# Kernel optimization log

Hardware: AMD Instinct MI355X
Metric: run time of the kernel (lower is better)

## Reference

```python
import jax, jax.numpy as jnp
import numpy as np

B, W, N, K = 8, 16, 40, 10
DN = DL = 128
DE = 128
H = 4
NEG_SLOPE = 0.2


def _build_graph():
    # per-graph ring adjacency: i -> (i+d) % N for d=1..K, in dense_to_sparse order (src-major, dst ascending)
    src0, dst0 = [], []
    for i in range(N):
        ds = sorted(((i + d) % N) for d in range(1, K + 1))
        src0 += [i] * K
        dst0 += ds
    src0 = np.asarray(src0)
    dst0 = np.asarray(dst0)
    G = B * W
    Epg = N * K
    offs = np.arange(G)[:, None] * N
    node_adj = np.stack([(src0[None] + offs).reshape(-1), (dst0[None] + offs).reshape(-1)])
    # line graph: for each node, pair every incoming edge with every outgoing edge (torch repeat/tile order)
    a0, a1, fe = [], [], []
    for num in range(N):
        inc = np.nonzero(dst0 == num)[0]
        out = np.nonzero(src0 == num)[0]
        a0.append(np.repeat(inc, out.size))
        a1.append(np.tile(out, inc.size))
        fe.append(np.full(inc.size * out.size, num))
    a0, a1, fe = np.concatenate(a0), np.concatenate(a1), np.concatenate(fe)
    keep = a0 != a1  # remove_self_loops (no-op here, kept for fidelity)
    a0, a1, fe = a0[keep], a1[keep], fe[keep]
    eoffs = np.arange(G)[:, None] * Epg
    edge_adj = np.stack([(a0[None] + eoffs).reshape(-1), (a1[None] + eoffs).reshape(-1)])
    edge_efea = (fe[None] + offs).reshape(-1)
    return node_adj, edge_adj, edge_efea


def setup_inputs() -> dict:
    key = jax.random.key(0)
    node_adj, edge_adj, edge_efea = _build_graph()
    Epg = N * K
    D1 = DN + DL
    ks = jax.random.split(key, 16)

    def lin(k, fi, fo):
        return jax.random.normal(k, (fi, fo), jnp.float32) / np.sqrt(fi).astype(np.float32)

    return dict(
        x_node=jax.random.normal(ks[0], (B, W, N, DN), jnp.float32),
        x_trace=jax.random.normal(ks[1], (B, W, Epg, DE), jnp.float32),
        x_log=jax.random.normal(ks[2], (B, W, N, DL), jnp.float32),
        node_adj=jnp.asarray(node_adj, jnp.int32),
        edge_adj=jnp.asarray(edge_adj, jnp.int32),
        edge_efea=jnp.asarray(edge_efea, jnp.int32),
        Wl1=lin(ks[3], D1, D1), bl1=jnp.zeros((D1,), jnp.float32),
        Wr1=lin(ks[4], D1, D1), br1=jnp.zeros((D1,), jnp.float32),
        We1=lin(ks[5], DE, D1), be1=jnp.zeros((D1,), jnp.float32),
        att1=jax.random.normal(ks[6], (H, D1 // H), jnp.float32) / np.sqrt(D1 // H).astype(np.float32),
        bias1=jnp.zeros((D1,), jnp.float32),
        Wl2=lin(ks[7], DE, DE), bl2=jnp.zeros((DE,), jnp.float32),
        Wr2=lin(ks[8], DE, DE), br2=jnp.zeros((DE,), jnp.float32),
        We2=lin(ks[9], D1, DE), be2=jnp.zeros((DE,), jnp.float32),
        att2=jax.random.normal(ks[10], (H, DE // H), jnp.float32) / np.sqrt(DE // H).astype(np.float32),
        bias2=jnp.zeros((DE,), jnp.float32),
    )


def _gatv2(x, edge_index, edge_attr, Wl, bl, Wr, br, We, be, att, bias, heads):
    """PyG GATv2Conv (eval mode, add_self_loops=False, concat heads)."""
    n = x.shape[0]
    HC = Wl.shape[1]
    C = HC // heads
    xl = (x @ Wl + bl).reshape(n, heads, C)  # source transform
    xr = (x @ Wr + br).reshape(n, heads, C)  # target transform
    src, dst = edge_index[0], edge_index[1]
    ea = (edge_attr @ We + be).reshape(-1, heads, C)
    m = jax.nn.leaky_relu(xl[src] + xr[dst] + ea, NEG_SLOPE)  # [E,H,C]
    logits = jnp.einsum('ehc,hc->eh', m, att)
    # segment softmax over incoming edges per target node
    mx = jax.ops.segment_max(logits, dst, num_segments=n)
    mx = jnp.where(jnp.isfinite(mx), mx, 0.0)
    ex = jnp.exp(logits - mx[dst])
    den = jax.ops.segment_sum(ex, dst, num_segments=n)
    alpha = ex / (den[dst] + 1e-16)
    out = jax.ops.segment_sum(alpha[:, :, None] * xl[src], dst, num_segments=n)  # [n,H,C]
    return out.reshape(n, HC) + bias


def reference(x_node, x_trace, x_log, node_adj, edge_adj, edge_efea,
              Wl1, bl1, Wr1, br1, We1, be1, att1, bias1,
              Wl2, bl2, Wr2, br2, We2, be2, att2, bias2):
    b, w, n, dn = x_node.shape
    dl = x_log.shape[-1]
    node = jnp.concatenate([x_node, x_log], axis=-1).reshape(-1, dn + dl)  # [G*N, Dn+Dl]
    trace = x_trace.reshape(-1, x_trace.shape[-1])                          # [G*Epg, De]
    node = _gatv2(node, node_adj, trace, Wl1, bl1, Wr1, br1, We1, be1, att1, bias1, H)
    trace = _gatv2(trace, edge_adj, node[edge_efea], Wl2, bl2, Wr2, br2, We2, be2, att2, bias2, H)
    x_node_o = node[:, :dn].reshape(b, w, n, dn)
    x_trace_o = trace.reshape(b, w, -1, trace.shape[-1])
    x_log_o = node[:, dn:].reshape(b, w, n, dl)
    return (x_node_o, x_trace_o, x_log_o)
```

## Files before the change

kernel.cpp:

```cpp
#include <hip/hip_runtime.h>
#include <hip/hip_bf16.h>

#define D1 256
#define DE 128
#define KDEG 10
#define LOG2E 1.44269504088896340736f

typedef __attribute__((ext_vector_type(8))) short short8;
typedef __attribute__((ext_vector_type(4))) float f32x4;

static inline int cdiv(size_t a, int b) { return (int)((a + b - 1) / b); }
static inline size_t al256(size_t x) { return (x + 255) & ~(size_t)255; }

__device__ __forceinline__ short f2b(float x) {
  __hip_bfloat16 h = __float2bfloat16(x);
  return *reinterpret_cast<short*>(&h);
}

__global__ __launch_bounds__(256) void k_setup(const float* __restrict__ xn,
                                               const float* __restrict__ xlg,
                                               const float* __restrict__ Wl1,
                                               const float* __restrict__ Wr1,
                                               const float* __restrict__ We1,
                                               const float* __restrict__ Wl2,
                                               const float* __restrict__ Wr2,
                                               const float* __restrict__ We2,
                                               const float* __restrict__ bl1,
                                               const float* __restrict__ br1,
                                               float* __restrict__ den1,
                                               int* __restrict__ cnt,
                                               float* __restrict__ X,
                                               short* __restrict__ WT12,
                                               short* __restrict__ We1T,
                                               short* __restrict__ W2T,
                                               short* __restrict__ We2T,
                                               float* __restrict__ blr1,
                                               int NN) {
  size_t idx = (size_t)blockIdx.x * 256 + threadIdx.x;
  size_t n;
  n = (size_t)NN * 4;       if (idx < n) { den1[idx] = 0.f; return; }           idx -= n;
  n = (size_t)NN;           if (idx < n) { cnt[idx] = 0; return; }              idx -= n;
  n = (size_t)NN * D1;
  if (idx < n) {
    int g = (int)(idx >> 8), c = (int)(idx & 255);
    X[idx] = (c < 128) ? xn[(size_t)g * 128 + c] : xlg[(size_t)g * 128 + (c - 128)];
    return;
  }
  idx -= n;
  n = 512 * 256;
  if (idx < n) {
    int nn = (int)(idx >> 8), k = (int)(idx & 255);
    float v = (nn < 256) ? Wl1[(size_t)k * 256 + nn] : Wr1[(size_t)k * 256 + (nn - 256)];
    WT12[idx] = f2b(v);
    return;
  }
  idx -= n;
  n = 256 * 128;
  if (idx < n) {
    int nn = (int)(idx >> 7), k = (int)(idx & 127);
    We1T[idx] = f2b(We1[(size_t)k * 256 + nn]);
    return;
  }
  idx -= n;
  n = 2 * 128 * 128;
  if (idx < n) {
    int half = (int)(idx >> 14);
    int r = (int)(idx & 16383);
    int nn = r >> 7, k = r & 127;
    const float* W = half ? Wr2 : Wl2;
    W2T[idx] = f2b(W[(size_t)k * 128 + nn]);
    return;
  }
  idx -= n;
  n = 128 * 256;
  if (idx < n) {
    int nn = (int)(idx >> 8), k = (int)(idx & 255);
    We2T[idx] = f2b(We2[(size_t)k * 128 + nn]);
    return;
  }
  idx -= n;
  n = 512;
  if (idx < n) blr1[idx] = (idx < 256) ? bl1[idx] : br1[idx - 256];
}

__global__ __launch_bounds__(256) void k_build_inc(const int* __restrict__ adj,
                                                   int* __restrict__ cnt,
                                                   int* __restrict__ inc, int NE) {
  int e = blockIdx.x * 256 + threadIdx.x;
  if (e >= NE) return;
  int dst = adj[NE + e];
  int slot = atomicAdd(&cnt[dst], 1);
  inc[dst * KDEG + slot] = e;
}

__global__ __launch_bounds__(256) void k_gemm_mfma(const float* __restrict__ A,
                                                   const short* __restrict__ WT,
                                                   const float* __restrict__ bias,
                                                   float* __restrict__ C,
                                                   int M, int K, int N) {
  __shared__ __align__(16) short As[128][40];
  __shared__ __align__(16) short Bs[128][40];
  const int tid = threadIdx.x;
  const int wave = tid >> 6, lane = tid & 63;
  const int quad = lane >> 4, l16 = lane & 15;
  const int m0 = blockIdx.y * 128, n0 = blockIdx.x * 128;
  const int wm = (wave & 1) * 64, wn = (wave >> 1) * 64;
  f32x4 acc[4][4] = {};
  for (int k0 = 0; k0 < K; k0 += 32) {
    #pragma unroll
    for (int s = 0; s < 2; ++s) {
      int ch = tid + s * 256;
      int r = ch >> 2, kc = (ch & 3) << 3;
      const float* src = &A[(size_t)(m0 + r) * K + (k0 + kc)];
      float4 v0 = *(const float4*)src;
      float4 v1 = *(const float4*)(src + 4);
      short8 t;
      t[0] = f2b(v0.x); t[1] = f2b(v0.y); t[2] = f2b(v0.z); t[3] = f2b(v0.w);
      t[4] = f2b(v1.x); t[5] = f2b(v1.y); t[6] = f2b(v1.z); t[7] = f2b(v1.w);
      *(short8*)&As[r][kc] = t;
      *(short8*)&Bs[r][kc] = *(const short8*)&WT[(size_t)(n0 + r) * K + (k0 + kc)];
    }
    __syncthreads();
    short8 af[4], bf[4];
    #pragma unroll
    for (int mt = 0; mt < 4; ++mt)
      af[mt] = *(const short8*)&As[wm + mt * 16 + l16][quad << 3];
    #pragma unroll
    for (int nt = 0; nt < 4; ++nt)
      bf[nt] = *(const short8*)&Bs[wn + nt * 16 + l16][quad << 3];
    #pragma unroll
    for (int mt = 0; mt < 4; ++mt)
      #pragma unroll
      for (int nt = 0; nt < 4; ++nt)
        acc[mt][nt] = __builtin_amdgcn_mfma_f32_16x16x32_bf16(
            af[mt], bf[nt], acc[mt][nt], 0, 0, 0);
    __syncthreads();
  }
  #pragma unroll
  for (int nt = 0; nt < 4; ++nt) {
    int col = n0 + wn + nt * 16 + l16;
    float bs = bias[col];
    #pragma unroll
    for (int mt = 0; mt < 4; ++mt) {
      int row = m0 + wm + mt * 16 + (quad << 2);
      #pragma unroll
      for (int r = 0; r < 4; ++r)
        C[(size_t)(row + r) * N + col] = acc[mt][nt][r] + bs;
    }
  }
}

__global__ __launch_bounds__(256) void k_gemm_mfma64(const float* __restrict__ A,
                                                     const short* __restrict__ WT,
                                                     const float* __restrict__ bias,
                                                     float* __restrict__ C,
                                                     int M, int K, int N) {
  __shared__ __align__(16) short As[64][40];
  __shared__ __align__(16) short Bs[64][40];
  const int tid = threadIdx.x;
  const int wave = tid >> 6, lane = tid & 63;
  const int quad = lane >> 4, l16 = lane & 15;
  const int m0 = blockIdx.y * 64, n0 = blockIdx.x * 64;
  const int wm = (wave & 1) * 32, wn = (wave >> 1) * 32;
  f32x4 acc[2][2] = {};
  for (int k0 = 0; k0 < K; k0 += 32) {
    {
      int r = tid >> 2, kc = (tid & 3) << 3;
      const float* src = &A[(size_t)(m0 + r) * K + (k0 + kc)];
      float4 v0 = *(const float4*)src;
      float4 v1 = *(const float4*)(src + 4);
      short8 t;
      t[0] = f2b(v0.x); t[1] = f2b(v0.y); t[2] = f2b(v0.z); t[3] = f2b(v0.w);
      t[4] = f2b(v1.x); t[5] = f2b(v1.y); t[6] = f2b(v1.z); t[7] = f2b(v1.w);
      *(short8*)&As[r][kc] = t;
      *(short8*)&Bs[r][kc] = *(const short8*)&WT[(size_t)(n0 + r) * K + (k0 + kc)];
    }
    __syncthreads();
    short8 af[2], bf[2];
    #pragma unroll
    for (int mt = 0; mt < 2; ++mt)
      af[mt] = *(const short8*)&As[wm + mt * 16 + l16][quad << 3];
    #pragma unroll
    for (int nt = 0; nt < 2; ++nt)
      bf[nt] = *(const short8*)&Bs[wn + nt * 16 + l16][quad << 3];
    #pragma unroll
    for (int mt = 0; mt < 2; ++mt)
      #pragma unroll
      for (int nt = 0; nt < 2; ++nt)
        acc[mt][nt] = __builtin_amdgcn_mfma_f32_16x16x32_bf16(
            af[mt], bf[nt], acc[mt][nt], 0, 0, 0);
    __syncthreads();
  }
  #pragma unroll
  for (int nt = 0; nt < 2; ++nt) {
    int col = n0 + wn + nt * 16 + l16;
    float bs = bias[col];
    #pragma unroll
    for (int mt = 0; mt < 2; ++mt) {
      int row = m0 + wm + mt * 16 + (quad << 2);
      #pragma unroll
      for (int r = 0; r < 4; ++r)
        C[(size_t)(row + r) * N + col] = acc[mt][nt][r] + bs;
    }
  }
}

__global__ __launch_bounds__(256) void k_logit1_lite(const int* __restrict__ adj,
                                                     const float* __restrict__ ea,
                                                     const float* __restrict__ xlr1,
                                                     const float* __restrict__ att1,
                                                     float* __restrict__ logit1,
                                                     float* __restrict__ den1,
                                                     int NE, int e0) {
  int eb = e0 + blockIdx.x * 8;
  int c = threadIdx.x;
  __shared__ int sd[8][2];
  if (c < 8)       sd[c][0] = adj[eb + c];
  else if (c < 16) sd[c - 8][1] = adj[NE + eb + (c - 8)];
  __syncthreads();
  int h = c >> 6;
  float att = att1[c] * LOG2E;
  #pragma unroll
  for (int j = 0; j < 8; ++j) {
    int s = sd[j][0], d = sd[j][1];
    float v = xlr1[(size_t)s * 512 + c] + xlr1[(size_t)d * 512 + 256 + c]
            + ea[(size_t)(eb - e0 + j) * D1 + c];
    v = (v > 0.f) ? v : 0.2f * v;
    float p = v * att;
    #pragma unroll
    for (int m = 32; m >= 1; m >>= 1) p += __shfl_xor(p, m, 64);
    if ((c & 63) == 0) {
      float ex = exp2f(p);
      logit1[(size_t)(eb + j) * 4 + h] = ex;
      atomicAdd(&den1[(size_t)d * 4 + h], ex);
    }
  }
}

__global__ __launch_bounds__(256) void k_agg1(const int* __restrict__ adj,
                                              const int* __restrict__ inc,
                                              const float* __restrict__ xlr1,
                                              const float* __restrict__ logit1,
                                              const float* __restrict__ den1,
                                              const float* __restrict__ bias1,
                                              float* __restrict__ nodeout,
                                              float* __restrict__ out_node,
                                              float* __restrict__ out_log) {
  int u = blockIdx.x, c = threadIdx.x;
  __shared__ int se[KDEG], ssrc[KDEG];
  __shared__ float slg[KDEG * 4];
  if (c < KDEG) se[c] = inc[u * KDEG + c];
  __syncthreads();
  if (c < KDEG) ssrc[c] = adj[se[c]];
  else if (c >= 64 && c < 64 + KDEG * 4) {
    int t = c - 64;
    slg[t] = logit1[(size_t)se[t >> 2] * 4 + (t & 3)];
  }
  __syncthreads();
  int h = c >> 6;
  float rden = 1.f / (den1[(size_t)u * 4 + h] + 1e-16f);
  float acc = 0.f;
  #pragma unroll
  for (int j = 0; j < KDEG; ++j)
    acc += slg[j * 4 + h] * xlr1[(size_t)ssrc[j] * 512 + c];
  float val = acc * rden + bias1[c];
  nodeout[(size_t)u * D1 + c] = val;
  if (c < 128) out_node[(size_t)u * 128 + c] = val;
  else         out_log[(size_t)u * 128 + (c - 128)] = val;
}

__global__ __launch_bounds__(256) void k_gat2_v3(const int* __restrict__ eadj,
                                                 const int* __restrict__ efea,
                                                 const float* __restrict__ xl2,
                                                 const float* __restrict__ nproj,
                                                 const float* __restrict__ att2,
                                                 const float* __restrict__ bias2,
                                                 float* trace,
                                                 int NL, int g0, int e0) {
  int gi = g0 + blockIdx.x;
  size_t le0 = (size_t)gi * 100;
  int t = threadIdx.x;
  __shared__ int ein[KDEG], eout[KDEG], nvs;
  __shared__ float xs[KDEG][132];
  __shared__ float rs[KDEG][132];
  __shared__ float as_[DE];
  __shared__ float exs[400];
  __shared__ float rdn[40];
  if (t < KDEG)          ein[t] = eadj[le0 + (size_t)t * KDEG];
  else if (t < 2 * KDEG) eout[t - KDEG] = eadj[(size_t)NL + le0 + (t - KDEG)];
  else if (t == 255)     nvs = efea[le0];
  __syncthreads();
  int nv = nvs;
  for (int s = t; s < 320; s += 256) {
    int j = s >> 5, q = (s & 31) << 2;
    *(float4*)&xs[j][q] = *(const float4*)&xl2[(size_t)(ein[j] - e0) * DE + q];
    float4 tr4 = *(const float4*)&trace[(size_t)eout[j] * DE + q];
    float4 ea4 = *(const float4*)&nproj[(size_t)nv * DE + q];
    float4 r;
    r.x = tr4.x + ea4.x; r.y = tr4.y + ea4.y;
    r.z = tr4.z + ea4.z; r.w = tr4.w + ea4.w;
    *(float4*)&rs[j][q] = r;
  }
  if (t < 32) {
    float4 a4 = *(const float4*)&att2[t << 2];
    float4 o;
    o.x = a4.x * LOG2E; o.y = a4.y * LOG2E;
    o.z = a4.z * LOG2E; o.w = a4.w * LOG2E;
    *(float4*)&as_[t << 2] = o;
  }
  __syncthreads();
  for (int s = t; s < 400; s += 256) {
    int h = s & 3;
    int j = s / 40;
    int o = (s - j * 40) >> 2;
    const float* xa = &xs[j][h << 5];
    const float* ra = &rs[o][h << 5];
    const float* aa = &as_[h << 5];
    float p = 0.f;
    #pragma unroll
    for (int i = 0; i < 32; i += 4) {
      float4 xv = *(const float4*)&xa[i];
      float4 rv = *(const float4*)&ra[i];
      float4 av = *(const float4*)&aa[i];
      float v;
      v = xv.x + rv.x; v = (v > 0.f) ? v : 0.2f * v; p += v * av.x;
      v = xv.y + rv.y; v = (v > 0.f) ? v : 0.2f * v; p += v * av.y;
      v = xv.z + rv.z; v = (v > 0.f) ? v : 0.2f * v; p += v * av.z;
      v = xv.w + rv.w; v = (v > 0.f) ? v : 0.2f * v; p += v * av.w;
    }
    exs[s] = exp2f(p);
  }
  __syncthreads();
  if (t < 40) {
    float d = 0.f;
    #pragma unroll
    for (int j = 0; j < KDEG; ++j) d += exs[(j * 10 + (t >> 2)) * 4 + (t & 3)];
    rdn[t] = 1.f / d;
  }
  __syncthreads();
  {
    int c = t & 127, h = c >> 5, oh = (t >> 7) * 5;
    float bsv = bias2[c];
    #pragma unroll
    for (int oo = 0; oo < 5; ++oo) {
      int o = oh + oo;
      float acc = 0.f;
      #pragma unroll
      for (int j = 0; j < KDEG; ++j)
        acc += exs[(j * 10 + o) * 4 + h] * xs[j][c];
      trace[(size_t)eout[o] * DE + c] = acc * rdn[o * 4 + h] + bsv;
    }
  }
}

extern "C" void kernel_launch(void* const* d_in, const int* in_sizes, int n_in,
                              void* d_out, int out_size, void* d_ws, size_t ws_size,
                              hipStream_t stream) {
  const float* x_node   = (const float*)d_in[0];
  const float* x_trace  = (const float*)d_in[1];
  const float* x_log    = (const float*)d_in[2];
  const int*   node_adj = (const int*)d_in[3];
  const int*   edge_adj = (const int*)d_in[4];
  const int*   edge_efea= (const int*)d_in[5];
  const float* Wl1 = (const float*)d_in[6];
  const float* bl1 = (const float*)d_in[7];
  const float* Wr1 = (const float*)d_in[8];
  const float* br1 = (const float*)d_in[9];
  const float* We1 = (const float*)d_in[10];
  const float* be1 = (const float*)d_in[11];
  const float* att1 = (const float*)d_in[12];
  const float* bias1 = (const float*)d_in[13];
  const float* Wl2 = (const float*)d_in[14];
  const float* bl2 = (const float*)d_in[15];
  const float* Wr2 = (const float*)d_in[16];
  const float* br2 = (const float*)d_in[17];
  const float* We2 = (const float*)d_in[18];
  const float* be2 = (const float*)d_in[19];
  const float* att2 = (const float*)d_in[20];
  const float* bias2 = (const float*)d_in[21];

  const int NN = in_sizes[0] / 128;
  const int NE = in_sizes[1] / 128;
  const int NL = in_sizes[5];

  size_t sz_xlr1  = al256((size_t)NN * 512 * 4);
  size_t sz_log1  = al256((size_t)NE * 4 * 4);
  size_t sz_den1  = al256((size_t)NN * 4 * 4);
  size_t sz_nproj = al256((size_t)NN * DE * 4);
  size_t sz_inc   = al256((size_t)NN * KDEG * 4);
  size_t sz_cnt   = al256((size_t)NN * 4);
  size_t sz_wt12  = al256((size_t)512 * 256 * 2);
  size_t sz_we1t  = al256((size_t)256 * 128 * 2);
  size_t sz_w2t   = al256((size_t)2 * 128 * 128 * 2);
  size_t sz_we2t  = al256((size_t)128 * 256 * 2);
  size_t sz_blr1  = al256(512 * 4);
  size_t tail = sz_xlr1 + sz_log1 + sz_den1 + sz_nproj + sz_inc + sz_cnt +
                sz_wt12 + sz_we1t + sz_w2t + sz_we2t + sz_blr1;
  char* tb = (char*)d_ws + ((ws_size - tail) & ~(size_t)255);
  float* xlr1   = (float*)tb;  tb += sz_xlr1;
  float* logit1 = (float*)tb;  tb += sz_log1;
  float* den1   = (float*)tb;  tb += sz_den1;
  float* nproj  = (float*)tb;  tb += sz_nproj;
  int*   inc    = (int*)tb;    tb += sz_inc;
  int*   cnt    = (int*)tb;    tb += sz_cnt;
  short* WT12   = (short*)tb;  tb += sz_wt12;
  short* We1T   = (short*)tb;  tb += sz_we1t;
  short* W2T    = (short*)tb;  tb += sz_w2t;
  short* We2T   = (short*)tb;  tb += sz_we2t;
  float* blr1   = (float*)tb;
  short* Wl2T = W2T, *Wr2T = W2T + (size_t)128 * 128;

  float* pool    = (float*)d_ws;
  float* X       = pool;
  float* nodeout = pool;
  size_t pool_avail = (size_t)((char*)d_ws + ((ws_size - tail) & ~(size_t)255) - (char*)d_ws);

  int p1 = 16, p2 = 16;
  for (int q = 1; q <= 16; q <<= 1)
    if (((size_t)NE / q) * D1 * 4 <= pool_avail) { p1 = q; break; }
  for (int q = 1; q <= 16; q <<= 1)
    if (((size_t)NE / q) * DE * 4 <= pool_avail) { p2 = q; break; }

  float* out_node  = (float*)d_out;
  float* out_trace = out_node + (size_t)NN * 128;
  float* out_log   = out_trace + (size_t)NE * 128;

  {
    size_t total = (size_t)NN * 5 + (size_t)NN * D1 + 512 * 256 + 256 * 128 +
                   2 * 128 * 128 + 128 * 256 + 512;
    k_setup<<<cdiv(total, 256), 256, 0, stream>>>(x_node, x_log, Wl1, Wr1, We1,
                                                  Wl2, Wr2, We2, bl1, br1,
                                                  den1, cnt, X, WT12, We1T, W2T,
                                                  We2T, blr1, NN);
  }
  k_build_inc<<<cdiv(NE, 256), 256, 0, stream>>>(node_adj, cnt, inc, NE);

  k_gemm_mfma<<<dim3(512 / 128, NN / 128), 256, 0, stream>>>(X, WT12, blr1, xlr1,
                                                             NN, D1, 512);
  {
    int ep = NE / p1;
    for (int q = 0; q < p1; ++q) {
      const float* At = x_trace + (size_t)q * ep * DE;
      k_gemm_mfma<<<dim3(D1 / 128, ep / 128), 256, 0, stream>>>(At, We1T, be1, pool,
                                                                ep, DE, D1);
      k_logit1_lite<<<ep / 8, 256, 0, stream>>>(node_adj, pool, xlr1, att1,
                                                logit1, den1, NE, q * ep);
    }
  }

  k_agg1<<<NN, 256, 0, stream>>>(node_adj, inc, xlr1, logit1, den1, bias1,
                                 nodeout, out_node, out_log);

  k_gemm_mfma64<<<dim3(DE / 64, NN / 64), 256, 0, stream>>>(nodeout, We2T, be2,
                                                            nproj, NN, D1, DE);
  k_gemm_mfma<<<dim3(DE / 128, NE / 128), 256, 0, stream>>>(x_trace, Wr2T, br2,
                                                            out_trace, NE, DE, DE);
  {
    int ep = NE / p2, gp = NN / p2;
    for (int q = 0; q < p2; ++q) {
      const float* At = x_trace + (size_t)q * ep * DE;
      k_gemm_mfma<<<dim3(DE / 128, ep / 128), 256, 0, stream>>>(At, Wl2T, bl2, pool,
                                                                ep, DE, DE);
      k_gat2_v3<<<gp, 256, 0, stream>>>(edge_adj, edge_efea, pool, nproj,
                                        att2, bias2, out_trace, NL, q * gp, q * ep);
    }
  }
}
```

Baseline: 253.1 us.

## Fuse all x_trace projections into one GEMM with fused layer-1 logit epilogue

The three GEMMs that read x_trace (We1, Wl2, Wr2) are merged into one GEMM with a concatenated 512-wide weight. Its epilogue computes the layer-1 attention logits, exp values and denominator atomics directly from the accumulators, and writes only the layer-2 projections to a full-size pool buffer. This removes the chunked launch loops, the separate logit kernel and the round-trip of the 256-wide edge projection through memory. In exchange it assumes the workspace can hold the full NE x 256 buffer, with no chunking fallback. It also switches the node GEMM to the 64-tile kernel and adds block-index swizzling.

Measured after the change: 256.3 us. Within noise of the previous version (+1.2%).

```diff
diff --git a/kernel.cpp b/kernel.cpp
--- a/kernel.cpp
+++ b/kernel.cpp
@@ -27,14 +27,17 @@
                                                const float* __restrict__ We2,
                                                const float* __restrict__ bl1,
                                                const float* __restrict__ br1,
+                                               const float* __restrict__ be1,
+                                               const float* __restrict__ bl2,
+                                               const float* __restrict__ br2,
                                                float* __restrict__ den1,
                                                int* __restrict__ cnt,
                                                float* __restrict__ X,
                                                short* __restrict__ WT12,
-                                               short* __restrict__ We1T,
-                                               short* __restrict__ W2T,
+                                               short* __restrict__ WTall,
                                                short* __restrict__ We2T,
                                                float* __restrict__ blr1,
+                                               float* __restrict__ bfull,
                                                int NN) {
   size_t idx = (size_t)blockIdx.x * 256 + threadIdx.x;
   size_t n;
@@ -55,20 +58,14 @@
     return;
   }
   idx -= n;
-  n = 256 * 128;
+  n = 512 * 128;
   if (idx < n) {
     int nn = (int)(idx >> 7), k = (int)(idx & 127);
-    We1T[idx] = f2b(We1[(size_t)k * 256 + nn]);
-    return;
-  }
-  idx -= n;
-  n = 2 * 128 * 128;
-  if (idx < n) {
-    int half = (int)(idx >> 14);
-    int r = (int)(idx & 16383);
-    int nn = r >> 7, k = r & 127;
-    const float* W = half ? Wr2 : Wl2;
-    W2T[idx] = f2b(W[(size_t)k * 128 + nn]);
+    float v;
+    if (nn < 256)      v = We1[(size_t)k * 256 + nn];
+    else if (nn < 384) v = Wl2[(size_t)k * 128 + (nn - 256)];
+    else               v = Wr2[(size_t)k * 128 + (nn - 384)];
+    WTall[idx] = f2b(v);
     return;
   }
   idx -= n;
@@ -80,7 +77,12 @@
   }
   idx -= n;
   n = 512;
-  if (idx < n) blr1[idx] = (idx < 256) ? bl1[idx] : br1[idx - 256];
+  if (idx < n) { blr1[idx] = (idx < 256) ? bl1[idx] : br1[idx - 256]; return; }
+  idx -= n;
+  n = 512;
+  if (idx < n) {
+    bfull[idx] = (idx < 256) ? be1[idx] : (idx < 384 ? bl2[idx - 256] : br2[idx - 384]);
+  }
 }
 
 __global__ __launch_bounds__(256) void k_build_inc(const int* __restrict__ adj,
@@ -91,63 +93,6 @@
   int dst = adj[NE + e];
   int slot = atomicAdd(&cnt[dst], 1);
   inc[dst * KDEG + slot] = e;
-}
-
-__global__ __launch_bounds__(256) void k_gemm_mfma(const float* __restrict__ A,
-                                                   const short* __restrict__ WT,
-                                                   const float* __restrict__ bias,
-                                                   float* __restrict__ C,
-                                                   int M, int K, int N) {
-  __shared__ __align__(16) short As[128][40];
-  __shared__ __align__(16) short Bs[128][40];
-  const int tid = threadIdx.x;
-  const int wave = tid >> 6, lane = tid & 63;
-  const int quad = lane >> 4, l16 = lane & 15;
-  const int m0 = blockIdx.y * 128, n0 = blockIdx.x * 128;
-  const int wm = (wave & 1) * 64, wn = (wave >> 1) * 64;
-  f32x4 acc[4][4] = {};
-  for (int k0 = 0; k0 < K; k0 += 32) {
-    #pragma unroll
-    for (int s = 0; s < 2; ++s) {
-      int ch = tid + s * 256;
-      int r = ch >> 2, kc = (ch & 3) << 3;
-      const float* src = &A[(size_t)(m0 + r) * K + (k0 + kc)];
-      float4 v0 = *(const float4*)src;
-      float4 v1 = *(const float4*)(src + 4);
-      short8 t;
-      t[0] = f2b(v0.x); t[1] = f2b(v0.y); t[2] = f2b(v0.z); t[3] = f2b(v0.w);
-      t[4] = f2b(v1.x); t[5] = f2b(v1.y); t[6] = f2b(v1.z); t[7] = f2b(v1.w);
-      *(short8*)&As[r][kc] = t;
-      *(short8*)&Bs[r][kc] = *(const short8*)&WT[(size_t)(n0 + r) * K + (k0 + kc)];
-    }
-    __syncthreads();
-    short8 af[4], bf[4];
-    #pragma unroll
-    for (int mt = 0; mt < 4; ++mt)
-      af[mt] = *(const short8*)&As[wm + mt * 16 + l16][quad << 3];
-    #pragma unroll
-    for (int nt = 0; nt < 4; ++nt)
-      bf[nt] = *(const short8*)&Bs[wn + nt * 16 + l16][quad << 3];
-    #pragma unroll
-    for (int mt = 0; mt < 4; ++mt)
-      #pragma unroll
-      for (int nt = 0; nt < 4; ++nt)
-        acc[mt][nt] = __builtin_amdgcn_mfma_f32_16x16x32_bf16(
-            af[mt], bf[nt], acc[mt][nt], 0, 0, 0);
-    __syncthreads();
-  }
-  #pragma unroll
-  for (int nt = 0; nt < 4; ++nt) {
-    int col = n0 + wn + nt * 16 + l16;
-    float bs = bias[col];
-    #pragma unroll
-    for (int mt = 0; mt < 4; ++mt) {
-      int row = m0 + wm + mt * 16 + (quad << 2);
-      #pragma unroll
-      for (int r = 0; r < 4; ++r)
-        C[(size_t)(row + r) * N + col] = acc[mt][nt][r] + bs;
-    }
-  }
 }
 
 __global__ __launch_bounds__(256) void k_gemm_mfma64(const float* __restrict__ A,
@@ -205,34 +150,108 @@
   }
 }
 
-__global__ __launch_bounds__(256) void k_logit1_lite(const int* __restrict__ adj,
-                                                     const float* __restrict__ ea,
-                                                     const float* __restrict__ xlr1,
-                                                     const float* __restrict__ att1,
-                                                     float* __restrict__ logit1,
-                                                     float* __restrict__ den1,
-                                                     int NE, int e0) {
-  int eb = e0 + blockIdx.x * 8;
-  int c = threadIdx.x;
-  __shared__ int sd[8][2];
-  if (c < 8)       sd[c][0] = adj[eb + c];
-  else if (c < 16) sd[c - 8][1] = adj[NE + eb + (c - 8)];
-  __syncthreads();
-  int h = c >> 6;
-  float att = att1[c] * LOG2E;
-  #pragma unroll
-  for (int j = 0; j < 8; ++j) {
-    int s = sd[j][0], d = sd[j][1];
-    float v = xlr1[(size_t)s * 512 + c] + xlr1[(size_t)d * 512 + 256 + c]
-            + ea[(size_t)(eb - e0 + j) * D1 + c];
-    v = (v > 0.f) ? v : 0.2f * v;
-    float p = v * att;
-    #pragma unroll
-    for (int m = 32; m >= 1; m >>= 1) p += __shfl_xor(p, m, 64);
-    if ((c & 63) == 0) {
-      float ex = exp2f(p);
-      logit1[(size_t)(eb + j) * 4 + h] = ex;
-      atomicAdd(&den1[(size_t)d * 4 + h], ex);
+__global__ __launch_bounds__(256) void k_gemm_fused(const float* __restrict__ A,
+                                                    const short* __restrict__ WT,
+                                                    const float* __restrict__ bfull,
+                                                    const float* __restrict__ att1,
+                                                    const int* __restrict__ adj,
+                                                    const float* __restrict__ xlr1,
+                                                    float* __restrict__ logit1,
+                                                    float* __restrict__ den1,
+                                                    float* __restrict__ pool2,
+                                                    int NE) {
+  const int K = 128;
+  __shared__ __align__(16) short As[128][40];
+  __shared__ __align__(16) short Bs[128][40];
+  const int tid = threadIdx.x;
+  const int wave = tid >> 6, lane = tid & 63;
+  const int quad = lane >> 4, l16 = lane & 15;
+  int bid = blockIdx.x;
+  int l = (bid & 7) * ((int)gridDim.x >> 3) + (bid >> 3);
+  const int n0 = (l & 3) << 7;
+  const int m0 = (l >> 2) << 7;
+  const int wm = (wave & 1) * 64, wn = (wave >> 1) * 64;
+  f32x4 acc[4][4] = {};
+  for (int k0 = 0; k0 < K; k0 += 32) {
+    #pragma unroll
+    for (int s = 0; s < 2; ++s) {
+      int ch = tid + s * 256;
+      int r = ch >> 2, kc = (ch & 3) << 3;
+      const float* src = &A[(size_t)(m0 + r) * K + (k0 + kc)];
+      float4 v0 = *(const float4*)src;
+      float4 v1 = *(const float4*)(src + 4);
+      short8 t;
+      t[0] = f2b(v0.x); t[1] = f2b(v0.y); t[2] = f2b(v0.z); t[3] = f2b(v0.w);
+      t[4] = f2b(v1.x); t[5] = f2b(v1.y); t[6] = f2b(v1.z); t[7] = f2b(v1.w);
+      *(short8*)&As[r][kc] = t;
+      *(short8*)&Bs[r][kc] = *(const short8*)&WT[(size_t)(n0 + r) * K + (k0 + kc)];
+    }
+    __syncthreads();
+    short8 af[4], bf[4];
+    #pragma unroll
+    for (int mt = 0; mt < 4; ++mt)
+      af[mt] = *(const short8*)&As[wm + mt * 16 + l16][quad << 3];
+    #pragma unroll
+    for (int nt = 0; nt < 4; ++nt)
+      bf[nt] = *(const short8*)&Bs[wn + nt * 16 + l16][quad << 3];
+    #pragma unroll
+    for (int mt = 0; mt < 4; ++mt)
+      #pragma unroll
+      for (int nt = 0; nt < 4; ++nt)
+        acc[mt][nt] = __builtin_amdgcn_mfma_f32_16x16x32_bf16(
+            af[mt], bf[nt], acc[mt][nt], 0, 0, 0);
+    __syncthreads();
+  }
+  if (n0 < 256) {
+    const int h = (n0 + wn) >> 6;
+    float attv[4], bev[4];
+    int cc[4];
+    #pragma unroll
+    for (int nt = 0; nt < 4; ++nt) {
+      int c = n0 + wn + nt * 16 + l16;
+      cc[nt] = c;
+      attv[nt] = att1[c] * LOG2E;
+      bev[nt] = bfull[c];
+    }
+    #pragma unroll
+    for (int mt = 0; mt < 4; ++mt) {
+      #pragma unroll
+      for (int r = 0; r < 4; ++r) {
+        int e = m0 + wm + mt * 16 + (quad << 2) + r;
+        int sN = adj[e], dN = adj[NE + e];
+        const float* xl = &xlr1[(size_t)sN * 512];
+        const float* xr = &xlr1[(size_t)dN * 512 + 256];
+        float p = 0.f;
+        #pragma unroll
+        for (int nt = 0; nt < 4; ++nt) {
+          float v = acc[mt][nt][r] + bev[nt] + xl[cc[nt]] + xr[cc[nt]];
+          v = (v > 0.f) ? v : 0.2f * v;
+          p += v * attv[nt];
+        }
+        p += __shfl_xor(p, 1, 64);
+        p += __shfl_xor(p, 2, 64);
+        p += __shfl_xor(p, 4, 64);
+        p += __shfl_xor(p, 8, 64);
+        if (l16 == 0) {
+          float ex = exp2f(p);
+          logit1[(size_t)e * 4 + h] = ex;
+          atomicAdd(&den1[(size_t)dN * 4 + h], ex);
+        }
+      }
+    }
+  } else {
+    #pragma unroll
+    for (int nt = 0; nt < 4; ++nt) {
+      int col = n0 + wn + nt * 16 + l16;
+      float bs = bfull[col];
+      int pcol = col - 256;
+      #pragma unroll
+      for (int mt = 0; mt < 4; ++mt) {
+        int row = m0 + wm + mt * 16 + (quad << 2);
+        #pragma unroll
+        for (int r = 0; r < 4; ++r)
+          pool2[(size_t)(row + r) * 256 + pcol] = acc[mt][nt][r] + bs;
+      }
     }
   }
 }
@@ -269,15 +288,15 @@
   else         out_log[(size_t)u * 128 + (c - 128)] = val;
 }
 
-__global__ __launch_bounds__(256) void k_gat2_v3(const int* __restrict__ eadj,
+__global__ __launch_bounds__(256) void k_gat2_v4(const int* __restrict__ eadj,
                                                  const int* __restrict__ efea,
-                                                 const float* __restrict__ xl2,
+                                                 const float* __restrict__ pool2,
                                                  const float* __restrict__ nproj,
                                                  const float* __restrict__ att2,
                                                  const float* __restrict__ bias2,
-                                                 float* trace,
-                                                 int NL, int g0, int e0) {
-  int gi = g0 + blockIdx.x;
+                                                 float* __restrict__ out_trace,
+                                                 int NL) {
+  int gi = blockIdx.x;
   size_t le0 = (size_t)gi * 100;
   int t = threadIdx.x;
   __shared__ int ein[KDEG], eout[KDEG], nvs;
@@ -293,8 +312,8 @@
   int nv = nvs;
   for (int s = t; s < 320; s += 256) {
     int j = s >> 5, q = (s & 31) << 2;
-    *(float4*)&xs[j][q] = *(const float4*)&xl2[(size_t)(ein[j] - e0) * DE + q];
-    float4 tr4 = *(const float4*)&trace[(size_t)eout[j] * DE + q];
+    *(float4*)&xs[j][q] = *(const float4*)&pool2[(size_t)ein[j] * 256 + q];
+    float4 tr4 = *(const float4*)&pool2[(size_t)eout[j] * 256 + 128 + q];
     float4 ea4 = *(const float4*)&nproj[(size_t)nv * DE + q];
     float4 r;
     r.x = tr4.x + ea4.x; r.y = tr4.y + ea4.y;
@@ -348,7 +367,7 @@
       #pragma unroll
       for (int j = 0; j < KDEG; ++j)
         acc += exs[(j * 10 + o) * 4 + h] * xs[j][c];
-      trace[(size_t)eout[o] * DE + c] = acc * rdn[o * 4 + h] + bsv;
+      out_trace[(size_t)eout[o] * DE + c] = acc * rdn[o * 4 + h] + bsv;
     }
   }
 }
@@ -383,86 +402,50 @@
   const int NE = in_sizes[1] / 128;
   const int NL = in_sizes[5];
 
-  size_t sz_xlr1  = al256((size_t)NN * 512 * 4);
-  size_t sz_log1  = al256((size_t)NE * 4 * 4);
-  size_t sz_den1  = al256((size_t)NN * 4 * 4);
-  size_t sz_nproj = al256((size_t)NN * DE * 4);
-  size_t sz_inc   = al256((size_t)NN * KDEG * 4);
-  size_t sz_cnt   = al256((size_t)NN * 4);
-  size_t sz_wt12  = al256((size_t)512 * 256 * 2);
-  size_t sz_we1t  = al256((size_t)256 * 128 * 2);
-  size_t sz_w2t   = al256((size_t)2 * 128 * 128 * 2);
-  size_t sz_we2t  = al256((size_t)128 * 256 * 2);
-  size_t sz_blr1  = al256(512 * 4);
-  size_t tail = sz_xlr1 + sz_log1 + sz_den1 + sz_nproj + sz_inc + sz_cnt +
-                sz_wt12 + sz_we1t + sz_w2t + sz_we2t + sz_blr1;
-  char* tb = (char*)d_ws + ((ws_size - tail) & ~(size_t)255);
-  float* xlr1   = (float*)tb;  tb += sz_xlr1;
-  float* logit1 = (float*)tb;  tb += sz_log1;
-  float* den1   = (float*)tb;  tb += sz_den1;
-  float* nproj  = (float*)tb;  tb += sz_nproj;
-  int*   inc    = (int*)tb;    tb += sz_inc;
-  int*   cnt    = (int*)tb;    tb += sz_cnt;
-  short* WT12   = (short*)tb;  tb += sz_wt12;
-  short* We1T   = (short*)tb;  tb += sz_we1t;
-  short* W2T    = (short*)tb;  tb += sz_w2t;
-  short* We2T   = (short*)tb;  tb += sz_we2t;
-  float* blr1   = (float*)tb;
-  short* Wl2T = W2T, *Wr2T = W2T + (size_t)128 * 128;
-
-  float* pool    = (float*)d_ws;
-  float* X       = pool;
-  float* nodeout = pool;
-  size_t pool_avail = (size_t)((char*)d_ws + ((ws_size - tail) & ~(size_t)255) - (char*)d_ws);
-
-  int p1 = 16, p2 = 16;
-  for (int q = 1; q <= 16; q <<= 1)
-    if (((size_t)NE / q) * D1 * 4 <= pool_avail) { p1 = q; break; }
-  for (int q = 1; q <= 16; q <<= 1)
-    if (((size_t)NE / q) * DE * 4 <= pool_avail) { p2 = q; break; }
+  char* p = (char*)d_ws;
+  float* pool2  = (float*)p; p += al256((size_t)NE * 256 * 4);
+  float* xlr1   = (float*)p; p += al256((size_t)NN * 512 * 4);
+  float* X      = (float*)p; p += al256((size_t)NN * D1 * 4);
+  float* nodeout= (float*)p; p += al256((size_t)NN * D1 * 4);
+  float* nproj  = (float*)p; p += al256((size_t)NN * DE * 4);
+  float* logit1 = (float*)p; p += al256((size_t)NE * 4 * 4);
+  float* den1   = (float*)p; p += al256((size_t)NN * 4 * 4);
+  int*   inc    = (int*)p;   p += al256((size_t)NN * KDEG * 4);
+  int*   cnt    = (int*)p;   p += al256((size_t)NN * 4);
+  short* WT12   = (short*)p; p += al256((size_t)512 * 256 * 2);
+  short* WTall  = (short*)p; p += al256((size_t)512 * 128 * 2);
+  short* We2T   = (short*)p; p += al256((size_t)128 * 256 * 2);
+  float* blr1   = (float*)p; p += al256(512 * 4);
+  float* bfull  = (float*)p; p += al256(512 * 4);
+  (void)ws_size;
 
   float* out_node  = (float*)d_out;
   float* out_trace = out_node + (size_t)NN * 128;
   float* out_log   = out_trace + (size_t)NE * 128;
 
   {
-    size_t total = (size_t)NN * 5 + (size_t)NN * D1 + 512 * 256 + 256 * 128 +
-                   2 * 128 * 128 + 128 * 256 + 512;
+    size_t total = (size_t)NN * 5 + (size_t)NN * D1 + 512 * 256 + 512 * 128 +
+                   128 * 256 + 512 + 512;
     k_setup<<<cdiv(total, 256), 256, 0, stream>>>(x_node, x_log, Wl1, Wr1, We1,
                                                   Wl2, Wr2, We2, bl1, br1,
-                                                  den1, cnt, X, WT12, We1T, W2T,
-                                                  We2T, blr1, NN);
+                                                  be1, bl2, br2,
+                                                  den1, cnt, X, WT12, WTall,
+                                                  We2T, blr1, bfull, NN);
   }
   k_build_inc<<<cdiv(NE, 256), 256, 0, stream>>>(node_adj, cnt, inc, NE);
 
-  k_gemm_mfma<<<dim3(512 / 128, NN / 128), 256, 0, stream>>>(X, WT12, blr1, xlr1,
+  k_gemm_mfma64<<<dim3(512 / 64, NN / 64), 256, 0, stream>>>(X, WT12, blr1, xlr1,
                                                              NN, D1, 512);
-  {
-    int ep = NE / p1;
-    for (int q = 0; q < p1; ++q) {
-      const float* At = x_trace + (size_t)q * ep * DE;
-      k_gemm_mfma<<<dim3(D1 / 128, ep / 128), 256, 0, stream>>>(At, We1T, be1, pool,
-                                                                ep, DE, D1);
-      k_logit1_lite<<<ep / 8, 256, 0, stream>>>(node_adj, pool, xlr1, att1,
-                                                logit1, den1, NE, q * ep);
-    }
-  }
+
+  k_gemm_fused<<<4 * (NE / 128), 256, 0, stream>>>(x_trace, WTall, bfull, att1,
+                                                   node_adj, xlr1, logit1, den1,
+                                                   pool2, NE);
 
   k_agg1<<<NN, 256, 0, stream>>>(node_adj, inc, xlr1, logit1, den1, bias1,
                                  nodeout, out_node, out_log);
 
   k_gemm_mfma64<<<dim3(DE / 64, NN / 64), 256, 0, stream>>>(nodeout, We2T, be2,
                                                             nproj, NN, D1, DE);
-  k_gemm_mfma<<<dim3(DE / 128, NE / 128), 256, 0, stream>>>(x_trace, Wr2T, br2,
-                                                            out_trace, NE, DE, DE);
-  {
-    int ep = NE / p2, gp = NN / p2;
-    for (int q = 0; q < p2; ++q) {
-      const float* At = x_trace + (size_t)q * ep * DE;
-      k_gemm_mfma<<<dim3(DE / 128, ep / 128), 256, 0, stream>>>(At, Wl2T, bl2, pool,
-                                                                ep, DE, DE);
-      k_gat2_v3<<<gp, 256, 0, stream>>>(edge_adj, edge_efea, pool, nproj,
-                                        att2, bias2, out_trace, NL, q * gp, q * ep);
-    }
-  }
-}
+  k_gat2_v4<<<NN, 256, 0, stream>>>(edge_adj, edge_efea, pool2, nproj,
+                                    att2, bias2, out_trace, NL);
+}
```
